# Optimization experiments

Measured on AMD Instinct MI355X. Metric: run time of the kernel, lower is better.

The kernel has to match this reference:

```python
import jax, jax.numpy as jnp
import numpy as np

KSIZE = 7
CUBIC_A = -0.5


def cubic_contribution(x, a=CUBIC_A):
    ax = jnp.abs(x)
    ax2 = ax * ax
    ax3 = ax * ax2
    cont_01 = ((a + 2) * ax3 - (a + 3) * ax2 + 1) * (ax <= 1).astype(x.dtype)
    cont_12 = (a * ax3 - 5 * a * ax2 + 8 * a * ax - 4 * a) * jnp.logical_and(ax > 1, ax <= 2).astype(x.dtype)
    return cont_01 + cont_12


def projective_grid(H, W, m, eps_x=0.0, eps_y=0.0):
    # Apply 3x3 homography m to pixel centers (x+eps_x, y+eps_y); returns (2, H*W).
    xs = jnp.arange(W, dtype=jnp.float32) + eps_x
    ys = jnp.arange(H, dtype=jnp.float32) + eps_y
    yy, xx = jnp.meshgrid(ys, xs, indexing='ij')
    xx = xx.ravel()
    yy = yy.ravel()
    X = m[0, 0] * xx + m[0, 1] * yy + m[0, 2]
    Y = m[1, 0] * xx + m[1, 1] * yy + m[1, 2]
    Z = m[2, 0] * xx + m[2, 1] * yy + m[2, 2]
    return jnp.stack((X / Z, Y / Z))


def setup_inputs() -> dict:
    key = jax.random.key(0)
    k1, k2 = jax.random.split(key)
    H = W = 1024
    N = H * W
    # near-identity homography (avoids degenerate perspective divide)
    m_inverse = jnp.eye(3, dtype=jnp.float32) + 0.001 * jax.random.normal(k1, (3, 3), dtype=jnp.float32)
    # source-space sampling positions, in-image range
    grid = jax.random.uniform(k2, (2, N), dtype=jnp.float32) * jnp.array([[W - 1.0], [H - 1.0]], dtype=jnp.float32)
    yi = jnp.arange(N, dtype=jnp.int32)
    return {"m_inverse": m_inverse, "grid": grid, "H": H, "W": W, "yi": yi}


def reference(m_inverse, grid, H, W, yi):
    K = KSIZE
    pad = K // 2
    offset = (K % 2) / 2  # 0.5 for odd kernels

    pos = grid + 1 - offset                      # (2, N)
    pos_frac = pos - jnp.floor(pos)              # (2, N)

    pl = projective_grid(H, W, m_inverse, eps_x=-0.5)
    pr = projective_grid(H, W, m_inverse, eps_x=0.5)
    pt = projective_grid(H, W, m_inverse, eps_y=-0.5)
    pb = projective_grid(H, W, m_inverse, eps_y=0.5)

    du = (pb - pt)[:, yi][:, :, None, None]      # (2, N, 1, 1)
    dv = (pr - pl)[:, yi][:, :, None, None]      # (2, N, 1, 1)

    # regularize |du| >= 1
    len_du = jnp.sqrt(du[0] ** 2 + du[1] ** 2)   # (N, 1, 1)
    mask_du = len_du < 1.0
    du = jnp.where(mask_du[None], du / len_du[None], du)
    len_du = jnp.where(mask_du, 1.0, len_du)

    # regularize |dv| >= 1
    len_dv = jnp.sqrt(dv[0] ** 2 + dv[1] ** 2)
    mask_dv = len_dv < 1.0
    dv = jnp.where(mask_dv[None], dv / len_dv[None], dv)
    len_dv = jnp.where(mask_dv, 1.0, len_dv)

    det = du[0] * dv[1] - du[1] * dv[0]          # (N, 1, 1)
    len_du = len_du * det
    len_dv = len_dv * det

    pos_w = jnp.linspace(pad - K + 1, pad, K).astype(jnp.float32) + offset  # (K,)
    pw = pos_frac[:, :, None] - pos_w[None, None, :]                        # (2, N, K)
    pos_wx = pw[0][:, None, :]                   # (N, 1, K)
    pos_wy = pw[1][:, :, None]                   # (N, K, 1)

    pos_wxp = (dv[1] * pos_wx - du[1] * pos_wy) / len_du  # (N, K, K)
    pos_wyp = (du[0] * pos_wy - dv[0] * pos_wx) / len_dv  # (N, K, K)

    x = du[0] * pos_wxp + du[1] * pos_wyp        # (N, K, K)
    y = dv[0] * pos_wxp + dv[1] * pos_wyp        # (N, K, K)

    weight = (cubic_contribution(x) * cubic_contribution(y)).reshape(x.shape[0], -1)  # (N, K*K)
    weight = weight / jnp.sum(weight, axis=-1, keepdims=True)
    return weight
```

## Files before the change

### kernel.cpp

```cpp
#include <hip/hip_runtime.h>

#define K 7
#define KK 49
#define BLK 256
#define TPP 4
#define PPB (BLK / TPP)
#define NW 13
#define CHUNK_F4 (PPB * KK / 4)

__device__ __forceinline__ float cubic_c(float x) {
    float ax = __builtin_fabsf(x);
    float t2 = __builtin_fmaxf(2.0f - ax, 0.0f);
    float t1 = __builtin_fmaxf(1.0f - ax, 0.0f);
    float r  = (t2 * t2) * __builtin_fmaf(0.5f, t2, -0.5f);
    return __builtin_fmaf(t1 * t1, __builtin_fmaf(-2.0f, t1, 1.0f), r);
}

__global__ __launch_bounds__(BLK, 8) void kest_kernel(
    const float* __restrict__ m,
    const float* __restrict__ grid,
    const int*   __restrict__ Wp,
    const int*   __restrict__ yi,
    float*       __restrict__ out,
    int N)
{
    __shared__ __align__(16) float lds[PPB * KK];

    const int tid  = threadIdx.x;
    const int sub  = tid & (TPP - 1);
    const int pixL = tid >> 2;
    const int i    = blockIdx.x * PPB + pixL;

    const float m00 = m[0], m01 = m[1], m02 = m[2];
    const float m10 = m[3], m11 = m[4], m12 = m[5];
    const float m20 = m[6], m21 = m[7], m22 = m[8];
    const int   W   = Wp[0];

    if (i < N) {
        const int j = yi[i];
        int yyI, xxI;
        if ((W & (W - 1)) == 0) {
            yyI = j >> (__ffs(W) - 1);
            xxI = j & (W - 1);
        } else {
            yyI = j / W;
            xxI = j - yyI * W;
        }
        const float xx = (float)xxI;
        const float yy = (float)yyI;

        const float X0 = m00 * xx + m01 * yy + m02;
        const float Y0 = m10 * xx + m11 * yy + m12;
        const float Z0 = m20 * xx + m21 * yy + m22;

        const float izy = 1.0f / (Z0 * Z0 - 0.25f * m21 * m21);
        float du0 = (m01 * Z0 - m21 * X0) * izy;
        float du1 = (m11 * Z0 - m21 * Y0) * izy;
        const float izx = 1.0f / (Z0 * Z0 - 0.25f * m20 * m20);
        float dv0 = (m00 * Z0 - m20 * X0) * izx;
        float dv1 = (m10 * Z0 - m20 * Y0) * izx;

        float len_du = __builtin_sqrtf(du0 * du0 + du1 * du1);
        if (len_du < 1.0f) {
            float r = 1.0f / len_du;
            du0 *= r; du1 *= r;
            len_du = 1.0f;
        }
        float len_dv = __builtin_sqrtf(dv0 * dv0 + dv1 * dv1);
        if (len_dv < 1.0f) {
            float r = 1.0f / len_dv;
            dv0 *= r; dv1 *= r;
            len_dv = 1.0f;
        }

        const float det  = du0 * dv1 - du1 * dv0;
        const float r_du = 1.0f / (len_du * det);
        const float r_dv = 1.0f / (len_dv * det);

        const float p1 = du0 * dv1, p2 = du1 * dv0;
        const float Axx = p1 * r_du - p2 * r_dv;
        const float Axy = du0 * du1 * (r_dv - r_du);
        const float Ayx = dv0 * dv1 * (r_du - r_dv);
        const float Ayy = p1 * r_dv - p2 * r_du;

        const float px  = grid[i]     + 0.5f;
        const float py  = grid[N + i] + 0.5f;
        const float fxc = (px - __builtin_floorf(px)) + 2.5f;
        const float fyc = (py - __builtin_floorf(py)) + 2.5f;

        float wv[NW];
        float wsum = 0.0f;
        int kx = sub, ky = 0;
#pragma unroll
        for (int qq = 0; qq < NW; ++qq) {
            const float wxv = fxc - (float)kx;
            const float wyv = fyc - (float)ky;
            const float x = __builtin_fmaf(Axx, wxv, Axy * wyv);
            const float y = __builtin_fmaf(Ayx, wxv, Ayy * wyv);
            float t = cubic_c(x) * cubic_c(y);
            if (qq == NW - 1 && sub >= 1) t = 0.0f;
            wv[qq] = t;
            wsum += t;
            kx += TPP;
            if (kx >= K) { kx -= K; ++ky; }
        }
        wsum += __shfl_xor(wsum, 1);
        wsum += __shfl_xor(wsum, 2);
        const float rs = 1.0f / wsum;

        float* p = &lds[pixL * KK + sub];
#pragma unroll
        for (int qq = 0; qq < NW; ++qq) {
            if (qq < NW - 1 || sub == 0)
                p[4 * qq] = wv[qq] * rs;
        }
    }
    __syncthreads();

    const long long baseF4 = (long long)blockIdx.x * CHUNK_F4;
    const long long limF4  = ((long long)N * KK) >> 2;
    const float4* src = (const float4*)lds;
    float4*       dst = (float4*)out + baseF4;
#pragma unroll
    for (int k = 0; k < 4; ++k) {
        const int t = tid + k * BLK;
        if (t < CHUNK_F4 && baseF4 + t < limF4) dst[t] = src[t];
    }
}

extern "C" void kernel_launch(void* const* d_in, const int* in_sizes, int n_in,
                              void* d_out, int out_size, void* d_ws, size_t ws_size,
                              hipStream_t stream) {
    const float* m    = (const float*)d_in[0];
    const float* grid = (const float*)d_in[1];
    const int*   Wp   = (const int*)d_in[3];
    const int*   yi   = (const int*)d_in[4];
    float*       out  = (float*)d_out;
    const int N = in_sizes[4];

    const int blocks = (N + PPB - 1) / PPB;
    kest_kernel<<<blocks, BLK, 0, stream>>>(m, grid, Wp, yi, out, N);
}
```

Before: 244.0 us.

## Use two threads per pixel and fast rcp/rsq intrinsics for weight kernel

Changes the work split from four to two threads per pixel, so each thread computes 25 of the 49 weights and the per-pixel setup is shared by fewer threads. Row and column indices are now compile-time constants chosen by the thread's sub-index, and the loads of the homography are moved inside the valid-pixel branch. Exact divisions and sqrt are replaced with hardware rcp/rsq approximations. In exchange each thread uses more registers, the occupancy hint drops to 6, and the approximate reciprocals may shift results slightly.

```diff
diff --git a/kernel.cpp b/kernel.cpp
--- a/kernel.cpp
+++ b/kernel.cpp
@@ -3,9 +3,9 @@
 #define K 7
 #define KK 49
 #define BLK 256
-#define TPP 4
+#define TPP 2
 #define PPB (BLK / TPP)
-#define NW 13
+#define NW 25
 #define CHUNK_F4 (PPB * KK / 4)
 
 __device__ __forceinline__ float cubic_c(float x) {
@@ -16,7 +16,7 @@
     return __builtin_fmaf(t1 * t1, __builtin_fmaf(-2.0f, t1, 1.0f), r);
 }
 
-__global__ __launch_bounds__(BLK, 8) void kest_kernel(
+__global__ __launch_bounds__(BLK, 6) void kest_kernel(
     const float* __restrict__ m,
     const float* __restrict__ grid,
     const int*   __restrict__ Wp,
@@ -28,15 +28,15 @@
 
     const int tid  = threadIdx.x;
     const int sub  = tid & (TPP - 1);
-    const int pixL = tid >> 2;
+    const int pixL = tid >> 1;
     const int i    = blockIdx.x * PPB + pixL;
 
-    const float m00 = m[0], m01 = m[1], m02 = m[2];
-    const float m10 = m[3], m11 = m[4], m12 = m[5];
-    const float m20 = m[6], m21 = m[7], m22 = m[8];
-    const int   W   = Wp[0];
+    if (i < N) {
+        const float m00 = m[0], m01 = m[1], m02 = m[2];
+        const float m10 = m[3], m11 = m[4], m12 = m[5];
+        const float m20 = m[6], m21 = m[7], m22 = m[8];
+        const int   W   = Wp[0];
 
-    if (i < N) {
         const int j = yi[i];
         int yyI, xxI;
         if ((W & (W - 1)) == 0) {
@@ -53,29 +53,25 @@
         const float Y0 = m10 * xx + m11 * yy + m12;
         const float Z0 = m20 * xx + m21 * yy + m22;
 
-        const float izy = 1.0f / (Z0 * Z0 - 0.25f * m21 * m21);
+        const float izy = __builtin_amdgcn_rcpf(Z0 * Z0 - 0.25f * m21 * m21);
         float du0 = (m01 * Z0 - m21 * X0) * izy;
         float du1 = (m11 * Z0 - m21 * Y0) * izy;
-        const float izx = 1.0f / (Z0 * Z0 - 0.25f * m20 * m20);
+        const float izx = __builtin_amdgcn_rcpf(Z0 * Z0 - 0.25f * m20 * m20);
         float dv0 = (m00 * Z0 - m20 * X0) * izx;
         float dv1 = (m10 * Z0 - m20 * Y0) * izx;
 
-        float len_du = __builtin_sqrtf(du0 * du0 + du1 * du1);
-        if (len_du < 1.0f) {
-            float r = 1.0f / len_du;
-            du0 *= r; du1 *= r;
-            len_du = 1.0f;
-        }
-        float len_dv = __builtin_sqrtf(dv0 * dv0 + dv1 * dv1);
-        if (len_dv < 1.0f) {
-            float r = 1.0f / len_dv;
-            dv0 *= r; dv1 *= r;
-            len_dv = 1.0f;
-        }
+        const float d2u = du0 * du0 + du1 * du1;
+        const float rlu = __builtin_amdgcn_rsqf(d2u);
+        float len_du = d2u * rlu;
+        if (len_du < 1.0f) { du0 *= rlu; du1 *= rlu; len_du = 1.0f; }
+        const float d2v = dv0 * dv0 + dv1 * dv1;
+        const float rlv = __builtin_amdgcn_rsqf(d2v);
+        float len_dv = d2v * rlv;
+        if (len_dv < 1.0f) { dv0 *= rlv; dv1 *= rlv; len_dv = 1.0f; }
 
         const float det  = du0 * dv1 - du1 * dv0;
-        const float r_du = 1.0f / (len_du * det);
-        const float r_dv = 1.0f / (len_dv * det);
+        const float r_du = __builtin_amdgcn_rcpf(len_du * det);
+        const float r_dv = __builtin_amdgcn_rcpf(len_dv * det);
 
         const float p1 = du0 * dv1, p2 = du1 * dv0;
         const float Axx = p1 * r_du - p2 * r_dv;
@@ -87,32 +83,31 @@
         const float py  = grid[N + i] + 0.5f;
         const float fxc = (px - __builtin_floorf(px)) + 2.5f;
         const float fyc = (py - __builtin_floorf(py)) + 2.5f;
+        const float subf = (float)sub;
 
         float wv[NW];
         float wsum = 0.0f;
-        int kx = sub, ky = 0;
 #pragma unroll
         for (int qq = 0; qq < NW; ++qq) {
-            const float wxv = fxc - (float)kx;
-            const float wyv = fyc - (float)ky;
+            const int c0 = (2 * qq) % 7,  c1 = (2 * qq + 1) % 7;
+            const int r0 = (2 * qq) / 7,  r1 = (2 * qq + 1) / 7;
+            const float wxv = __builtin_fmaf(subf, (float)(c0 - c1), fxc - (float)c0);
+            const float wyv = __builtin_fmaf(subf, (float)(r0 - r1), fyc - (float)r0);
             const float x = __builtin_fmaf(Axx, wxv, Axy * wyv);
             const float y = __builtin_fmaf(Ayx, wxv, Ayy * wyv);
             float t = cubic_c(x) * cubic_c(y);
-            if (qq == NW - 1 && sub >= 1) t = 0.0f;
+            if (qq == NW - 1) t = sub ? 0.0f : t;
             wv[qq] = t;
             wsum += t;
-            kx += TPP;
-            if (kx >= K) { kx -= K; ++ky; }
         }
         wsum += __shfl_xor(wsum, 1);
-        wsum += __shfl_xor(wsum, 2);
-        const float rs = 1.0f / wsum;
+        const float rs = __builtin_amdgcn_rcpf(wsum);
 
         float* p = &lds[pixL * KK + sub];
 #pragma unroll
         for (int qq = 0; qq < NW; ++qq) {
             if (qq < NW - 1 || sub == 0)
-                p[4 * qq] = wv[qq] * rs;
+                p[2 * qq] = wv[qq] * rs;
         }
     }
     __syncthreads();
@@ -122,7 +117,7 @@
     const float4* src = (const float4*)lds;
     float4*       dst = (float4*)out + baseF4;
 #pragma unroll
-    for (int k = 0; k < 4; ++k) {
+    for (int k = 0; k < 7; ++k) {
         const int t = tid + k * BLK;
         if (t < CHUNK_F4 && baseF4 + t < limF4) dst[t] = src[t];
     }
```

After: 219.8 us. 1.11x faster.
